# Performance work log

Hardware: AMD Instinct MI355X
Metric: run time of the kernel (lower is better)

## Reference

```python
import jax, jax.numpy as jnp
import numpy as np

B, S, D = 2, 2048, 1024
H = 16            # attention heads
KVH = 4           # key/value heads
G = H // KVH      # group_size = 4
HD = D // H       # head_dim = 64
ROPE_THETA = 10000.0


def rope(x):
    # x: [B, S, D]; interleaved-pair rotary embedding over full last dim
    d = x.shape[-1]
    inv_freq = 1.0 / (ROPE_THETA ** (jnp.arange(0, d, 2, dtype=jnp.float32) / d))  # [d/2]
    ang = jnp.arange(x.shape[1], dtype=jnp.float32)[:, None] * inv_freq[None, :]   # [S, d/2]
    cos, sin = jnp.cos(ang), jnp.sin(ang)
    x1, x2 = x[..., 0::2], x[..., 1::2]
    r1 = x1 * cos - x2 * sin
    r2 = x1 * sin + x2 * cos
    out = jnp.stack([r1, r2], axis=-1).reshape(x.shape)
    return out


def setup_inputs() -> dict:
    key = jax.random.key(0)
    kx, kq, kk, kv = jax.random.split(key, 4)
    x = jax.random.normal(kx, (B, S, D), dtype=jnp.float32)
    # mark last 256 positions of batch element 1 as padding via NaN
    x = x.at[1, S - 256:, :].set(jnp.nan)
    scale = 1.0 / np.sqrt(D)
    Wq = jax.random.normal(kq, (D, D), dtype=jnp.float32) * scale
    Wk = jax.random.normal(kk, (D, D // G), dtype=jnp.float32) * scale
    Wv = jax.random.normal(kv, (D, D // G), dtype=jnp.float32) * scale
    return {"x": x, "Wq": Wq, "Wk": Wk, "Wv": Wv}


def reference(x, Wq, Wk, Wv):
    pad = jnp.isnan(x)                      # [B,S,D]
    x = jnp.where(pad, 0.0, x)
    key_pad = jnp.any(pad, axis=-1)         # [B,S] True = padded token

    q = x @ Wq                              # [B,S,D]
    k = jnp.repeat(x @ Wk, G, axis=-1)      # grouped KV, repeat_interleave -> [B,S,D]
    v = jnp.repeat(x @ Wv, G, axis=-1)

    q = rope(q)
    k = rope(k)

    def split_heads(t):
        return t.reshape(B, S, H, HD).transpose(0, 2, 1, 3)  # [B,H,S,HD]

    q, k, v = split_heads(q), split_heads(k), split_heads(v)

    scores = jnp.einsum('bhqd,bhkd->bhqk', q, k) / np.sqrt(HD)
    causal = jnp.tril(jnp.ones((S, S), dtype=bool))
    allow = causal[None, None, :, :] & (~key_pad)[:, None, None, :]
    scores = jnp.where(allow, scores, -1e9)
    attn = jax.nn.softmax(scores, axis=-1)
    out = jnp.einsum('bhqk,bhkd->bhqd', attn, v)
    return out.transpose(0, 2, 1, 3).reshape(B, S, D)
```

## Files before the change

kernel.cpp:

```cpp
#include <hip/hip_runtime.h>
#include <hip/hip_bf16.h>
#include <math.h>

typedef unsigned short u16;
typedef unsigned int u32;
typedef __bf16 bf16x8 __attribute__((ext_vector_type(8)));
typedef float fx4 __attribute__((ext_vector_type(4)));

#define MFMA16(a, b, c) __builtin_amdgcn_mfma_f32_16x16x32_bf16(a, b, c, 0, 0, 0)

static constexpr int Bb = 2, Ss = 2048, Dd = 1024, Hh = 16, DKV = 256;
static constexpr int NQKV = 1536;
static constexpr int ROWS = Bb * Ss;
static constexpr float L2T_OVER = 0.0259525632f;
static constexpr float SC2 = 0.18033688f;
static constexpr int PSTR = 76;

__device__ __forceinline__ u16 f2bf(float f) {
    union { float f; u32 i; } v; v.f = f;
    u32 u = v.i;
    return (u16)((u + 0x7FFFu + ((u >> 16) & 1u)) >> 16);
}
__device__ __forceinline__ u16 bfr(float f) {
    return (u16)((__float_as_uint(f) + 0x8000u) >> 16);
}

__device__ __forceinline__ void gl16(const u16* g, u16* l) {
    __builtin_amdgcn_global_load_lds(
        (const __attribute__((address_space(1))) void*)g,
        (__attribute__((address_space(3))) void*)l, 16, 0, 0);
}

template <int CTRL>
__device__ __forceinline__ float dppf(float x) {
    return __int_as_float(
        __builtin_amdgcn_mov_dpp(__float_as_int(x), CTRL, 0xF, 0xF, true));
}
__device__ __forceinline__ float rsum16(float x) {
    x += dppf<0xB1>(x);
    x += dppf<0x4E>(x);
    x += dppf<0x124>(x);
    x += dppf<0x128>(x);
    return x;
}

__global__ void pre_kernel(const float* __restrict__ x, const float* __restrict__ Wq,
                           const float* __restrict__ Wk, const float* __restrict__ Wv,
                           u16* __restrict__ xc, u32* __restrict__ kpb,
                           u16* __restrict__ wAll) {
    __shared__ u16 tile[32][33];
    __shared__ int flag;
    int bid = blockIdx.x, t = threadIdx.x;
    if (bid < 4096) {
        int row = bid;
        if (t == 0) flag = 0;
        __syncthreads();
        float4 d = *(const float4*)(x + (size_t)row * Dd + t * 4);
        int any = 0;
        float a0 = d.x, a1 = d.y, a2 = d.z, a3 = d.w;
        if ((__float_as_uint(a0) & 0x7FFFFFFFu) > 0x7F800000u) { a0 = 0.f; any = 1; }
        if ((__float_as_uint(a1) & 0x7FFFFFFFu) > 0x7F800000u) { a1 = 0.f; any = 1; }
        if ((__float_as_uint(a2) & 0x7FFFFFFFu) > 0x7F800000u) { a2 = 0.f; any = 1; }
        if ((__float_as_uint(a3) & 0x7FFFFFFFu) > 0x7F800000u) { a3 = 0.f; any = 1; }
        if (any) atomicOr(&flag, 1);
        uint2 o;
        o.x = (u32)f2bf(a0) | ((u32)f2bf(a1) << 16);
        o.y = (u32)f2bf(a2) | ((u32)f2bf(a3) << 16);
        *(uint2*)(xc + (size_t)row * Dd + t * 4) = o;
        __syncthreads();
        if (t == 0 && flag) {
            int b = row >> 11, s = row & (Ss - 1);
            atomicOr(&kpb[b * 64 + (s >> 5)], 1u << (s & 31));
        }
        return;
    }
    const float* in; u16* out; int C, bx, by;
    if (bid < 5120) { int i = bid - 4096; in = Wq; out = wAll; C = Dd; bx = i & 31; by = i >> 5; }
    else if (bid < 5376) { int i = bid - 5120; in = Wk; out = wAll + (size_t)Dd * Dd; C = DKV; bx = i & 7; by = i >> 3; }
    else { int i = bid - 5376; in = Wv; out = wAll + (size_t)1280 * Dd; C = DKV; bx = i & 7; by = i >> 3; }
    int c0 = bx * 32, r0 = by * 32;
    int tx = t & 31, ty = t >> 5;
    for (int i = 0; i < 32; i += 8)
        tile[ty + i][tx] = f2bf(in[(size_t)(r0 + ty + i) * C + c0 + tx]);
    __syncthreads();
    for (int i = 0; i < 32; i += 8)
        out[(size_t)(c0 + ty + i) * Dd + r0 + tx] = tile[tx][ty + i];
}

__global__ __launch_bounds__(256) void gemm_qkv(
    const u16* __restrict__ A, const u16* __restrict__ Bt, u16* __restrict__ C) {
    __shared__ __align__(16) u16 As[2][128 * 32];
    __shared__ __align__(16) u16 Bs[2][64 * 32];
    int t = threadIdx.x, w = t >> 6, lane = t & 63;
    int l15 = lane & 15, quad = lane >> 4;
    int col0 = blockIdx.x * 64, row0 = blockIdx.y * 128;
    int wm = w >> 1, wn = w & 1;
    fx4 acc[4][2];
#pragma unroll
    for (int i = 0; i < 4; ++i)
#pragma unroll
        for (int j = 0; j < 2; ++j) acc[i][j] = (fx4){0.f, 0.f, 0.f, 0.f};

    auto stage = [&](int kb, int buf) {
#pragma unroll
        for (int i = 0; i < 2; ++i) {
            int slot = i * 256 + t;
            int row = slot >> 2, p = slot & 3, g = p ^ ((row >> 1) & 3);
            gl16(A + (size_t)(row0 + row) * Dd + kb * 32 + g * 8,
                 &As[buf][(i * 256 + w * 64) * 8]);
        }
        {
            int row = t >> 2, p = t & 3, g = p ^ ((row >> 1) & 3);
            gl16(Bt + (size_t)(col0 + row) * Dd + kb * 32 + g * 8,
                 &Bs[buf][(w * 64) * 8]);
        }
    };

    stage(0, 0);
    int buf = 0;
    for (int kb = 0; kb < 32; ++kb) {
        __syncthreads();
        if (kb + 1 < 32) stage(kb + 1, buf ^ 1);
        bf16x8 af[4], bfr2[2];
#pragma unroll
        for (int mi = 0; mi < 4; ++mi) {
            int row = wm * 64 + mi * 16 + l15;
            af[mi] = *(const bf16x8*)(&As[buf][row * 32 + ((quad ^ ((row >> 1) & 3)) * 8)]);
        }
#pragma unroll
        for (int ni = 0; ni < 2; ++ni) {
            int row = wn * 32 + ni * 16 + l15;
            bfr2[ni] = *(const bf16x8*)(&Bs[buf][row * 32 + ((quad ^ ((row >> 1) & 3)) * 8)]);
        }
#pragma unroll
        for (int mi = 0; mi < 4; ++mi)
#pragma unroll
            for (int ni = 0; ni < 2; ++ni)
                acc[mi][ni] = MFMA16(af[mi], bfr2[ni], acc[mi][ni]);
        buf ^= 1;
    }
#pragma unroll
    for (int mi = 0; mi < 4; ++mi) {
        int rbase = row0 + wm * 64 + mi * 16 + quad * 4;
#pragma unroll
        for (int ni = 0; ni < 2; ++ni) {
            int ccol = col0 + wn * 32 + ni * 16 + l15;
#pragma unroll
            for (int r = 0; r < 4; ++r)
                C[(size_t)(rbase + r) * NQKV + ccol] = f2bf(acc[mi][ni][r]);
        }
    }
}

__global__ void post_kernel(const u16* __restrict__ qkv, u16* __restrict__ kr,
                            u16* __restrict__ vtb) {
    __shared__ u16 tile[32][33];
    int bid = blockIdx.x, t = threadIdx.x;
    if (bid < 4096) {
        int row = bid;
        float pos = (float)(row & (Ss - 1));
        float kv = __uint_as_float(((u32)qkv[(size_t)row * NQKV + Dd + t]) << 16);
        float j0 = (float)(2 * t), j1 = j0 + 1.0f;
        float f0 = exp2f(-j0 * L2T_OVER), f1 = exp2f(-j1 * L2T_OVER);
        float s0, c0, s1, c1;
        sincosf(pos * f0, &s0, &c0);
        sincosf(pos * f1, &s1, &c1);
        float r0 = kv * (c0 - s0), r1 = kv * (s0 + c0);
        float r2 = kv * (c1 - s1), r3 = kv * (s1 + c1);
        uint2 o;
        o.x = (u32)f2bf(r0) | ((u32)f2bf(r1) << 16);
        o.y = (u32)f2bf(r2) | ((u32)f2bf(r3) << 16);
        *(uint2*)(kr + (size_t)row * Dd + t * 4) = o;
        return;
    }
    int i = bid - 4096;
    int b = i >> 9, by = (i & 511) >> 3, bx = i & 7;
    int c0 = bx * 32, r0 = by * 32;
    int tx = t & 31, ty = t >> 5;
    for (int k = 0; k < 32; k += 8)
        tile[ty + k][tx] = qkv[(size_t)(b * Ss + r0 + ty + k) * NQKV + 1280 + c0 + tx];
    __syncthreads();
    for (int k = 0; k < 32; k += 8)
        vtb[(size_t)(b * DKV + c0 + ty + k) * Ss + r0 + tx] = tile[tx][ty + k];
}

__device__ __forceinline__ bf16x8 ropeFrag(uint4 raw, float pos, float jbase) {
    u32 W[4] = {raw.x, raw.y, raw.z, raw.w};
    union { u32 u[4]; bf16x8 v; } o;
#pragma unroll
    for (int c = 0; c < 4; ++c) {
        float x0 = __uint_as_float(W[c] << 16);
        float x1 = __uint_as_float(W[c] & 0xFFFF0000u);
        float f = exp2f(-(jbase + (float)c) * L2T_OVER);
        float sn, cs;
        sincosf(pos * f, &sn, &cs);
        float r0 = x0 * cs - x1 * sn, r1 = x0 * sn + x1 * cs;
        o.u[c] = (u32)f2bf(r0) | ((u32)f2bf(r1) << 16);
    }
    return o.v;
}

__global__ __launch_bounds__(256) void attn_kernel(
    const u16* __restrict__ qkv, const u16* __restrict__ kr,
    const u16* __restrict__ vt, const u32* __restrict__ kpb,
    float* __restrict__ out) {
    __shared__ __align__(16) u16 Ks[2][64 * 64];
    __shared__ __align__(16) u16 Vs[2][16 * 64];
    __shared__ __align__(16) u16 Ps[4][16 * PSTR];

    int t = threadIdx.x, w = t >> 6, lane = t & 63;
    int l15 = lane & 15, quad = lane >> 4;
    int bid = blockIdx.x;
    int u = bid >> 5, g = u >> 3, i = u & 7;
    int tile = (g == 0) ? (31 - i) : (g == 1) ? (16 + i) : (g == 2) ? (15 - i) : i;
    int hh = bid & 31, b = hh >> 4, h = hh & 15;
    int q0 = tile * 64;
    int nkb = tile + 1;

    int pos = q0 + w * 16 + l15;
    const u16* qp = qkv + (size_t)(b * Ss + pos) * NQKV + h * 64;
    float jb = (float)(h * 32 + quad * 4);
    bf16x8 qf0 = ropeFrag(*(const uint4*)(qp + quad * 8), (float)pos, jb);
    bf16x8 qf1 = ropeFrag(*(const uint4*)(qp + 32 + quad * 8), (float)pos, jb + 16.f);

    u32 pw_all = kpb[b * 64 + lane];

    auto stageK = [&](int k0, int buf) {
#pragma unroll
        for (int i2 = 0; i2 < 2; ++i2) {
            int row = i2 * 32 + w * 8 + (lane >> 3);
            int gg = (lane & 7) ^ (row & 7);
            gl16(kr + (size_t)(b * Ss + k0 + row) * Dd + h * 64 + gg * 8,
                 &Ks[buf][(i2 * 32 + w * 8) * 64]);
        }
    };
    auto stageV = [&](int k0, int buf) {
        if (w < 2) {
            int row = w * 8 + (lane >> 3);
            int gg = (lane & 7) ^ (row & 7);
            gl16(vt + (size_t)(b * DKV + h * 16 + row) * Ss + k0 + gg * 8,
                 &Vs[buf][(w * 8) * 64]);
        }
    };

    float l_lane[4] = {0.f, 0.f, 0.f, 0.f};
    fx4 oacc = (fx4){0.f, 0.f, 0.f, 0.f};

    stageK(0, 0);
    stageV(0, 0);
    int buf = 0;
    const int qrb = q0 + w * 16 + quad * 4;
    const int qmin = q0 + w * 16;

    for (int kb = 0; kb < nkb; ++kb) {
        int k0 = kb * 64;
        __syncthreads();
        if (kb + 1 < nkb) { stageK(k0 + 64, buf ^ 1); stageV(k0 + 64, buf ^ 1); }

        fx4 s[4];
#pragma unroll
        for (int tt = 0; tt < 4; ++tt) {
            const u16* kb_ = &Ks[buf][(tt * 16 + l15) * 64];
            bf16x8 kf0 = *(const bf16x8*)(kb_ + ((quad ^ (l15 & 7)) * 8));
            bf16x8 kf1 = *(const bf16x8*)(kb_ + (((quad + 4) ^ (l15 & 7)) * 8));
            fx4 z = (fx4){0.f, 0.f, 0.f, 0.f};
            fx4 a = MFMA16(qf0, kf0, z);
            s[tt] = MFMA16(qf1, kf1, a);
        }

        u32 pw0 = (u32)__shfl((int)pw_all, 2 * kb, 64);
        u32 pw1 = (u32)__shfl((int)pw_all, 2 * kb + 1, 64);
        bool fast = (k0 + 63 <= qmin) & ((pw0 | pw1) == 0u);

        float e[4][4];
        if (fast) {
#pragma unroll
            for (int tt = 0; tt < 4; ++tt)
#pragma unroll
                for (int r = 0; r < 4; ++r)
                    e[tt][r] = exp2f(fmaf(s[tt][r], SC2, -32.f));
        } else {
            u32 padb[4];
#pragma unroll
            for (int tt = 0; tt < 4; ++tt)
                padb[tt] = ((tt & 2 ? pw1 : pw0) >> ((tt * 16 + l15) & 31)) & 1u;
#pragma unroll
            for (int r = 0; r < 4; ++r) {
                int qq = qrb + r;
#pragma unroll
                for (int tt = 0; tt < 4; ++tt) {
                    float ee = exp2f(fmaf(s[tt][r], SC2, -32.f));
                    e[tt][r] = (k0 + tt * 16 + l15 <= qq && !padb[tt]) ? ee : 0.f;
                }
            }
        }

#pragma unroll
        for (int r = 0; r < 4; ++r) {
            l_lane[r] += (e[0][r] + e[1][r]) + (e[2][r] + e[3][r]);
            int prow = (quad * 4 + r) * PSTR + l15;
            Ps[w][prow + 0] = bfr(e[0][r]);
            Ps[w][prow + 16] = bfr(e[1][r]);
            Ps[w][prow + 32] = bfr(e[2][r]);
            Ps[w][prow + 48] = bfr(e[3][r]);
        }

#pragma unroll
        for (int hh2 = 0; hh2 < 2; ++hh2) {
            bf16x8 vf = *(const bf16x8*)(&Vs[buf][l15 * 64 + (((quad + 4 * hh2) ^ (l15 & 7)) * 8)]);
            bf16x8 pf = *(const bf16x8*)(&Ps[w][l15 * PSTR + hh2 * 32 + quad * 8]);
            oacc = MFMA16(pf, vf, oacc);
        }
        buf ^= 1;
    }

#pragma unroll
    for (int r = 0; r < 4; ++r) {
        float l_row = rsum16(l_lane[r]);
        float a = oacc[r] / l_row;
        float4 o4 = {a, a, a, a};
        *(float4*)(out + (size_t)(b * Ss + qrb + r) * Dd + h * 64 + l15 * 4) = o4;
    }
}

extern "C" void kernel_launch(void* const* d_in, const int* in_sizes, int n_in,
                              void* d_out, int out_size, void* d_ws, size_t ws_size,
                              hipStream_t stream) {
    const float* x = (const float*)d_in[0];
    const float* Wq = (const float*)d_in[1];
    const float* Wk = (const float*)d_in[2];
    const float* Wv = (const float*)d_in[3];
    float* out = (float*)d_out;

    char* ws = (char*)d_ws;
    const size_t SZ_XC = (size_t)ROWS * Dd * 2;
    const size_t SZ_KPB = 4096;
    const size_t SZ_WALL = (size_t)NQKV * Dd * 2;
    const size_t SZ_QKV = (size_t)ROWS * NQKV * 2;

    size_t off = 0;
    u16* xc = (u16*)(ws + off);
    u16* krope = (u16*)(ws + off); off += SZ_XC;
    u32* kpb = (u32*)(ws + off); off += SZ_KPB;
    u16* wAll = (u16*)(ws + off);
    u16* vtb = (u16*)(ws + off); off += SZ_WALL;
    u16* qkv = (u16*)(ws + off); off += SZ_QKV;
    (void)ws_size; (void)in_sizes; (void)n_in; (void)out_size;

    hipMemsetAsync(kpb, 0, 2 * 64 * 4, stream);
    pre_kernel<<<5632, 256, 0, stream>>>(x, Wq, Wk, Wv, xc, kpb, wAll);
    gemm_qkv<<<dim3(NQKV / 64, ROWS / 128), 256, 0, stream>>>(xc, wAll, qkv);
    post_kernel<<<5120, 256, 0, stream>>>(qkv, krope, vtb);
    attn_kernel<<<1024, 256, 0, stream>>>(qkv, krope, vtb, kpb, out);
}
```

Measured before the change: 152.0 us.

## Split attention KV range across blocks with atomic partial sums and normalize pass

Splits each query tile's key range into chunks of 8 key blocks so long causal rows are processed by several blocks, which balances work and raises block count from 1024 to 2560. Partial unnormalized outputs and row sums are combined with float atomics into a workspace, and a new normalization kernel divides and writes the final output. V fragments are now loaded directly from global memory into registers instead of being staged through shared memory. This adds a memset, atomic traffic, and an extra kernel launch in exchange for better load balance. Combining partials without a per-chunk max is valid only because the exponent uses a fixed offset rather than a running max.

```diff
diff --git a/kernel.cpp b/kernel.cpp
--- a/kernel.cpp
+++ b/kernel.cpp
@@ -203,19 +203,23 @@
 __global__ __launch_bounds__(256) void attn_kernel(
     const u16* __restrict__ qkv, const u16* __restrict__ kr,
     const u16* __restrict__ vt, const u32* __restrict__ kpb,
-    float* __restrict__ out) {
+    float* __restrict__ O16, float* __restrict__ Lsum) {
     __shared__ __align__(16) u16 Ks[2][64 * 64];
-    __shared__ __align__(16) u16 Vs[2][16 * 64];
     __shared__ __align__(16) u16 Ps[4][16 * PSTR];
 
     int t = threadIdx.x, w = t >> 6, lane = t & 63;
     int l15 = lane & 15, quad = lane >> 4;
     int bid = blockIdx.x;
-    int u = bid >> 5, g = u >> 3, i = u & 7;
-    int tile = (g == 0) ? (31 - i) : (g == 1) ? (16 + i) : (g == 2) ? (15 - i) : i;
+    int u = bid >> 5;
+    int tile, c;
+    if (u < 32)      { tile = 24 + (u & 7); c = u >> 3; }
+    else if (u < 56) { tile = 16 + ((u - 32) & 7); c = (u - 32) >> 3; }
+    else if (u < 72) { tile = 8 + ((u - 56) & 7); c = (u - 56) >> 3; }
+    else             { tile = u - 72; c = 0; }
     int hh = bid & 31, b = hh >> 4, h = hh & 15;
     int q0 = tile * 64;
-    int nkb = tile + 1;
+    int kb0 = c * 8;
+    int kbe = min(kb0 + 8, tile + 1);
 
     int pos = q0 + w * 16 + l15;
     const u16* qp = qkv + (size_t)(b * Ss + pos) * NQKV + h * 64;
@@ -225,6 +229,8 @@
 
     u32 pw_all = kpb[b * 64 + lane];
 
+    const u16* vrow = vt + (size_t)(b * DKV + h * 16 + l15) * Ss;
+
     auto stageK = [&](int k0, int buf) {
 #pragma unroll
         for (int i2 = 0; i2 < 2; ++i2) {
@@ -234,28 +240,22 @@
                  &Ks[buf][(i2 * 32 + w * 8) * 64]);
         }
     };
-    auto stageV = [&](int k0, int buf) {
-        if (w < 2) {
-            int row = w * 8 + (lane >> 3);
-            int gg = (lane & 7) ^ (row & 7);
-            gl16(vt + (size_t)(b * DKV + h * 16 + row) * Ss + k0 + gg * 8,
-                 &Vs[buf][(w * 8) * 64]);
-        }
-    };
 
     float l_lane[4] = {0.f, 0.f, 0.f, 0.f};
     fx4 oacc = (fx4){0.f, 0.f, 0.f, 0.f};
 
-    stageK(0, 0);
-    stageV(0, 0);
+    stageK(kb0 * 64, 0);
     int buf = 0;
     const int qrb = q0 + w * 16 + quad * 4;
     const int qmin = q0 + w * 16;
 
-    for (int kb = 0; kb < nkb; ++kb) {
+    for (int kb = kb0; kb < kbe; ++kb) {
         int k0 = kb * 64;
         __syncthreads();
-        if (kb + 1 < nkb) { stageK(k0 + 64, buf ^ 1); stageV(k0 + 64, buf ^ 1); }
+        if (kb + 1 < kbe) stageK(k0 + 64, buf ^ 1);
+
+        bf16x8 vf0 = *(const bf16x8*)(vrow + k0 + quad * 8);
+        bf16x8 vf1 = *(const bf16x8*)(vrow + k0 + 32 + quad * 8);
 
         fx4 s[4];
 #pragma unroll
@@ -305,22 +305,36 @@
             Ps[w][prow + 48] = bfr(e[3][r]);
         }
 
-#pragma unroll
-        for (int hh2 = 0; hh2 < 2; ++hh2) {
-            bf16x8 vf = *(const bf16x8*)(&Vs[buf][l15 * 64 + (((quad + 4 * hh2) ^ (l15 & 7)) * 8)]);
-            bf16x8 pf = *(const bf16x8*)(&Ps[w][l15 * PSTR + hh2 * 32 + quad * 8]);
-            oacc = MFMA16(pf, vf, oacc);
+        {
+            bf16x8 pf0 = *(const bf16x8*)(&Ps[w][l15 * PSTR + quad * 8]);
+            bf16x8 pf1 = *(const bf16x8*)(&Ps[w][l15 * PSTR + 32 + quad * 8]);
+            oacc = MFMA16(pf0, vf0, oacc);
+            oacc = MFMA16(pf1, vf1, oacc);
         }
         buf ^= 1;
     }
 
+    size_t obase = (size_t)hh * Ss;
 #pragma unroll
     for (int r = 0; r < 4; ++r) {
         float l_row = rsum16(l_lane[r]);
-        float a = oacc[r] / l_row;
-        float4 o4 = {a, a, a, a};
-        *(float4*)(out + (size_t)(b * Ss + qrb + r) * Dd + h * 64 + l15 * 4) = o4;
-    }
+        int q = qrb + r;
+        atomicAdd(&O16[(obase + q) * 16 + l15], oacc[r]);
+        if (l15 == 0) atomicAdd(&Lsum[obase + q], l_row);
+    }
+}
+
+__global__ void norm_kernel(const float* __restrict__ O16, const float* __restrict__ Lsum,
+                            float* __restrict__ out) {
+    int idx = blockIdx.x * 256 + threadIdx.x;
+    int d4 = idx & 255;
+    int row = idx >> 8;
+    int h = d4 >> 4, f = d4 & 15;
+    int b = row >> 11, s = row & (Ss - 1);
+    size_t o = (size_t)(b * 16 + h) * Ss + s;
+    float a = O16[o * 16 + f] / Lsum[o];
+    float4 o4 = {a, a, a, a};
+    *(float4*)(out + (size_t)row * Dd + d4 * 4) = o4;
 }
 
 extern "C" void kernel_launch(void* const* d_in, const int* in_sizes, int n_in,
@@ -337,6 +351,8 @@
     const size_t SZ_KPB = 4096;
     const size_t SZ_WALL = (size_t)NQKV * Dd * 2;
     const size_t SZ_QKV = (size_t)ROWS * NQKV * 2;
+    const size_t SZ_O16 = (size_t)32 * Ss * 16 * 4;
+    const size_t SZ_L = (size_t)32 * Ss * 4;
 
     size_t off = 0;
     u16* xc = (u16*)(ws + off);
@@ -345,11 +361,15 @@
     u16* wAll = (u16*)(ws + off);
     u16* vtb = (u16*)(ws + off); off += SZ_WALL;
     u16* qkv = (u16*)(ws + off); off += SZ_QKV;
+    float* O16 = (float*)(ws + off); off += SZ_O16;
+    float* Ls = (float*)(ws + off); off += SZ_L;
     (void)ws_size; (void)in_sizes; (void)n_in; (void)out_size;
 
     hipMemsetAsync(kpb, 0, 2 * 64 * 4, stream);
+    hipMemsetAsync(O16, 0, SZ_O16 + SZ_L, stream);
     pre_kernel<<<5632, 256, 0, stream>>>(x, Wq, Wk, Wv, xc, kpb, wAll);
     gemm_qkv<<<dim3(NQKV / 64, ROWS / 128), 256, 0, stream>>>(xc, wAll, qkv);
     post_kernel<<<5120, 256, 0, stream>>>(qkv, krope, vtb);
-    attn_kernel<<<1024, 256, 0, stream>>>(qkv, krope, vtb, kpb, out);
-}
+    attn_kernel<<<2560, 256, 0, stream>>>(qkv, krope, vtb, kpb, O16, Ls);
+    norm_kernel<<<4096, 256, 0, stream>>>(O16, Ls, out);
+}
```

After: 160.0 us. +5.3%, slower.
